# Performance work log

Measured on AMD Instinct MI355X. Metric: run time of the kernel, lower is better.

Reference implementation:

```python
import jax, jax.numpy as jnp
import numpy as np

RF = 500_000   # total full-rec atoms (rows)
F1 = 256       # input feature dim
NF = 128       # n_feat output dim
RA = 50_000    # number of residues (segments) = res_index.max()+1
LN_EPS = 1e-5


def setup_inputs() -> dict:
    key = jax.random.key(0)
    ks = jax.random.split(key, 5)
    full_rec_data = jax.random.normal(ks[0], (RF, F1), dtype=jnp.float32)
    # ensure segment RA-1 appears so amax()+1 == RA deterministically
    res_index = jax.random.randint(ks[1], (RF,), 0, RA, dtype=jnp.int32)
    res_index = res_index.at[0].set(RA - 1)
    W_feat = jax.random.normal(ks[2], (F1, NF), dtype=jnp.float32) * 0.05
    b_feat = jnp.zeros((NF,), dtype=jnp.float32)
    ln_gamma = jnp.ones((NF,), dtype=jnp.float32)
    ln_beta = jnp.zeros((NF,), dtype=jnp.float32)
    W_atn = jax.random.normal(ks[3], (F1, 1), dtype=jnp.float32) * 0.05
    b_atn = jnp.zeros((1,), dtype=jnp.float32)
    return {
        "full_rec_data": full_rec_data,
        "W_feat": W_feat,
        "b_feat": b_feat,
        "ln_gamma": ln_gamma,
        "ln_beta": ln_beta,
        "W_atn": W_atn,
        "b_atn": b_atn,
        "res_index": res_index,
        "n_feat": NF,
    }


def _layer_norm(x, gamma, beta):
    mu = jnp.mean(x, axis=-1, keepdims=True)
    var = jnp.mean(jnp.square(x - mu), axis=-1, keepdims=True)
    return (x - mu) * jax.lax.rsqrt(var + LN_EPS) * gamma + beta


def reference(full_rec_data, W_feat, b_feat, ln_gamma, ln_beta, W_atn, b_atn, res_index, n_feat):
    # NormAndLinear: LayerNorm(Linear(leaky_relu(x)))
    act = jax.nn.leaky_relu(full_rec_data, negative_slope=0.01)   # (Rf, F1)
    feat = _layer_norm(act @ W_feat + b_feat, ln_gamma, ln_beta)  # (Rf, NF)
    # attention logits (Rf, 1), globally max-stabilized as in the original
    atn = act @ W_atn + b_atn
    atn = jnp.exp(atn - jnp.max(atn))
    # segment softmax denominator; RA is static (res_index.amax()+1)
    atn_sum = jax.ops.segment_sum(atn, res_index, num_segments=RA)  # (Ra, 1)
    atn = atn / atn_sum[res_index]                                  # (Rf, 1)
    # weighted scatter-add pooling -> (Ra, NF)
    return jax.ops.segment_sum(feat * atn, res_index, num_segments=RA)
```

## Files before the change

### kernel.cpp

```cpp
#include <hip/hip_runtime.h>
#include <hip/hip_bf16.h>

#define RFn 500000
#define F1n 256
#define NFn 128
#define RAn 50000
#define LN_EPSn 1e-5f
#define RECB 256
#define LTS 272
#define NTILE (RFn / 16)
#define NWAVE 4096
#define ROWPAD 1040
#define BUFB (16 * ROWPAD)
#define SCB 256
#define SCG ((RAn + SCB - 1) / SCB)

typedef float f32x4 __attribute__((ext_vector_type(4)));
typedef short short8 __attribute__((ext_vector_type(8)));

__device__ __forceinline__ short f2bf(float f) {
  __hip_bfloat16 h = __float2bfloat16(f);
  return __builtin_bit_cast(short, h);
}

__device__ __forceinline__ void gload_lds16(const void* g, void* l) {
  __builtin_amdgcn_global_load_lds(
      (const __attribute__((address_space(1))) void*)g,
      (__attribute__((address_space(3))) void*)l, 16, 0, 0);
}

__global__ void prep_kernel(const float* __restrict__ Wf, short* __restrict__ frag) {
  int p = blockIdx.x * blockDim.x + threadIdx.x;
  if (p >= 4096) return;
  int f = p >> 6, l = p & 63;
  int s = f >> 3, c = f & 7;
  int col = c * 16 + (l & 15);
  int k0 = s * 32 + ((l >> 4) << 3);
  short8 v;
#pragma unroll
  for (int i = 0; i < 8; ++i) v[i] = f2bf(Wf[(k0 + i) * NFn + col]);
  *(short8*)(frag + (size_t)p * 8) = v;
}

__global__ void hist_kernel(const int* __restrict__ ri, int* __restrict__ hist) {
  int i = blockIdx.x * 256 + threadIdx.x;
  if (i < RFn) atomicAdd(&hist[ri[i]], 1);
}

__global__ __launch_bounds__(256) void scanA_kernel(const int* __restrict__ hist,
                                                    int* __restrict__ T,
                                                    int* __restrict__ bsum) {
  __shared__ int ls[256];
  const int t = threadIdx.x, idx = blockIdx.x * 256 + t;
  const int v = (idx < RAn) ? hist[idx] : 0;
  ls[t] = v;
  __syncthreads();
  for (int off = 1; off < 256; off <<= 1) {
    int add = (t >= off) ? ls[t - off] : 0;
    __syncthreads();
    ls[t] += add;
    __syncthreads();
  }
  if (idx < RAn) T[idx] = ls[t] - v;
  if (t == 255) bsum[blockIdx.x] = ls[255];
}

__global__ __launch_bounds__(256) void scanB_kernel(int* __restrict__ bsum,
                                                    int* __restrict__ boff) {
  __shared__ int ls[256];
  const int t = threadIdx.x;
  const int v = (t < SCG) ? bsum[t] : 0;
  ls[t] = v;
  __syncthreads();
  for (int off = 1; off < 256; off <<= 1) {
    int add = (t >= off) ? ls[t - off] : 0;
    __syncthreads();
    ls[t] += add;
    __syncthreads();
  }
  if (t < SCG) boff[t] = ls[t] - v;
}

__global__ __launch_bounds__(256) void scanC_kernel(const int* __restrict__ T,
                                                    const int* __restrict__ boff,
                                                    int* __restrict__ rowstart,
                                                    int* __restrict__ cursor) {
  const int idx = blockIdx.x * 256 + threadIdx.x;
  if (idx < RAn) {
    int v = T[idx] + boff[blockIdx.x];
    rowstart[idx] = v;
    cursor[idx] = v;
  }
  if (idx == 0) rowstart[RAn] = RFn;
}

__global__ void scatter_kernel(const int* __restrict__ ri, int* __restrict__ cursor,
                               int* __restrict__ inv) {
  int i = blockIdx.x * 256 + threadIdx.x;
  if (i < RFn) inv[i] = atomicAdd(&cursor[ri[i]], 1);
}

__global__ __launch_bounds__(64) void featw2_kernel(
    const float* __restrict__ X, const short* __restrict__ fragWS,
    const float* __restrict__ Wa, const float* __restrict__ ba,
    const float* __restrict__ bfeat, const float* __restrict__ gamma,
    const float* __restrict__ beta, const int* __restrict__ inv,
    char* __restrict__ buf, float* __restrict__ wbuf) {
  __shared__ __attribute__((aligned(16))) char lds[2 * BUFB];

  const int lane = threadIdx.x;
  const int colb = lane & 15;
  const int kg = lane >> 4;

  float g_r[8], be_r[8], bi_r[8];
#pragma unroll
  for (int c = 0; c < 8; ++c) {
    int col = c * 16 + colb;
    g_r[c] = gamma[col];
    be_r[c] = beta[col];
    bi_r[c] = bfeat[col];
  }
  const float batn = ba[0];

  int t = blockIdx.x;
  {
    const float* xr = X + (size_t)t * 16 * F1n;
#pragma unroll
    for (int r = 0; r < 16; ++r)
      gload_lds16(xr + r * F1n + lane * 4, &lds[r * ROWPAD]);
  }
  int cur = 0;

  while (true) {
    const int tn = t + NWAVE;
    const bool more = (tn < NTILE);

    asm volatile("s_waitcnt vmcnt(0)" ::: "memory");
    __builtin_amdgcn_sched_barrier(0);

    if (more) {
      const float* xr = X + (size_t)tn * 16 * F1n;
      char* db = &lds[(cur ^ 1) * BUFB];
#pragma unroll
      for (int r = 0; r < 16; ++r)
        gload_lds16(xr + r * F1n + lane * 4, db + r * ROWPAD);
    }

    const char* A = &lds[cur * BUFB];
    f32x4 acc[8];
#pragma unroll
    for (int c = 0; c < 8; ++c) acc[c] = (f32x4)(0.0f);
    float logit = 0.f;

#pragma unroll
    for (int s = 0; s < 8; ++s) {
      short8 bfr[8];
#pragma unroll
      for (int c = 0; c < 8; ++c)
        bfr[c] = *(const short8*)(fragWS + (((s * 8 + c) * 64 + lane) * 8));
      const float4 wa0 = *(const float4*)(Wa + s * 32 + kg * 8);
      const float4 wa1 = *(const float4*)(Wa + s * 32 + kg * 8 + 4);
      const float4 x0 = *(const float4*)(A + colb * ROWPAD + s * 128 + kg * 32);
      const float4 x1 = *(const float4*)(A + colb * ROWPAD + s * 128 + kg * 32 + 16);
      float a0 = fmaxf(x0.x, 0.01f * x0.x);
      float a1 = fmaxf(x0.y, 0.01f * x0.y);
      float a2 = fmaxf(x0.z, 0.01f * x0.z);
      float a3 = fmaxf(x0.w, 0.01f * x0.w);
      float a4 = fmaxf(x1.x, 0.01f * x1.x);
      float a5 = fmaxf(x1.y, 0.01f * x1.y);
      float a6 = fmaxf(x1.z, 0.01f * x1.z);
      float a7 = fmaxf(x1.w, 0.01f * x1.w);
      logit += a0 * wa0.x + a1 * wa0.y + a2 * wa0.z + a3 * wa0.w +
               a4 * wa1.x + a5 * wa1.y + a6 * wa1.z + a7 * wa1.w;
      short8 af;
      af[0] = f2bf(a0); af[1] = f2bf(a1); af[2] = f2bf(a2); af[3] = f2bf(a3);
      af[4] = f2bf(a4); af[5] = f2bf(a5); af[6] = f2bf(a6); af[7] = f2bf(a7);
#pragma unroll
      for (int c = 0; c < 8; ++c)
        acc[c] = __builtin_amdgcn_mfma_f32_16x16x32_bf16(af, bfr[c], acc[c], 0, 0, 0);
    }

    char* lt = &lds[cur * BUFB];
    {
      float lg = logit;
      lg += __shfl_xor(lg, 16);
      lg += __shfl_xor(lg, 32);
      const float wexp = __expf(lg + batn);
      if (lane < 16) wbuf[inv[t * 16 + colb]] = wexp;

      float w4[4];
#pragma unroll
      for (int reg = 0; reg < 4; ++reg) w4[reg] = __shfl(wexp, kg * 4 + reg);

      float s1v[4] = {0.f, 0.f, 0.f, 0.f}, s2v[4] = {0.f, 0.f, 0.f, 0.f};
#pragma unroll
      for (int c = 0; c < 8; ++c)
#pragma unroll
        for (int reg = 0; reg < 4; ++reg) {
          float v = acc[c][reg] + bi_r[c];
          acc[c][reg] = v;
          s1v[reg] += v;
          s2v[reg] += v * v;
        }
#pragma unroll
      for (int off = 1; off <= 8; off <<= 1)
#pragma unroll
        for (int reg = 0; reg < 4; ++reg) {
          s1v[reg] += __shfl_xor(s1v[reg], off);
          s2v[reg] += __shfl_xor(s2v[reg], off);
        }
#pragma unroll
      for (int reg = 0; reg < 4; ++reg) {
        float mu = s1v[reg] * (1.0f / NFn);
        float var = s2v[reg] * (1.0f / NFn) - mu * mu;
        float rs = rsqrtf(var + LN_EPSn);
#pragma unroll
        for (int c = 0; c < 8; ++c) {
          float feat = (acc[c][reg] - mu) * rs * g_r[c] + be_r[c];
          ((short*)lt)[(kg * 4 + reg) * (LTS / 2) + c * 16 + colb] =
              f2bf(feat * w4[reg]);
        }
      }
    }

    {
      const int r = lane >> 2, j = lane & 3;
      char* dst = buf + (size_t)inv[t * 16 + r] * RECB;
#pragma unroll
      for (int i = 0; i < 4; ++i) {
        int4 v = *(const int4*)&lt[r * LTS + j * 64 + i * 16];
        *(int4*)(dst + j * 64 + i * 16) = v;
      }
    }

    if (!more) break;
    cur ^= 1;
    t = tn;
  }
}

__global__ __launch_bounds__(256) void reduce_kernel(
    const char* __restrict__ buf, const float* __restrict__ wbuf,
    const int* __restrict__ rowstart, float* __restrict__ out) {
  const int lane = threadIdx.x & 63;
  const int seg = blockIdx.x * 4 + (threadIdx.x >> 6);
  if (seg >= RAn) return;
  const int rb = rowstart[seg], re = rowstart[seg + 1];
  float a0 = 0.f, a1 = 0.f, wsum = 0.f;
  for (int p = rb; p < re; ++p) {
    const char* rec = buf + (size_t)p * RECB;
    unsigned v = *(const unsigned*)(rec + lane * 4);
    a0 += __builtin_bit_cast(float, v << 16);
    a1 += __builtin_bit_cast(float, v & 0xffff0000u);
    wsum += wbuf[p];
  }
  float2 o;
  if (re > rb) {
    o.x = a0 / wsum;
    o.y = a1 / wsum;
  } else {
    o.x = 0.f;
    o.y = 0.f;
  }
  *(float2*)(out + (size_t)seg * NFn + lane * 2) = o;
}

__global__ __launch_bounds__(256) void main_atomic(
    const float* __restrict__ X, const short* __restrict__ fragWS,
    const float* __restrict__ Wa, const float* __restrict__ ba,
    const float* __restrict__ bfeat, const float* __restrict__ gamma,
    const float* __restrict__ beta, const int* __restrict__ res_index,
    float* __restrict__ Nacc, float* __restrict__ D) {
  __shared__ short sB[4096 * 8];
  const int tid = threadIdx.x;
  {
    const int4* src = (const int4*)fragWS;
    int4* dst = (int4*)sB;
#pragma unroll 4
    for (int i = tid; i < 4096; i += 256) dst[i] = src[i];
  }
  __syncthreads();
  const int lane = tid & 63;
  const int wv = tid >> 6;
  const int rowbase = blockIdx.x * 128 + wv * 32;
  const int colb = lane & 15;
  const int kg = lane >> 4;
  float g_r[8], be_r[8], bi_r[8];
#pragma unroll
  for (int c = 0; c < 8; ++c) {
    int col = c * 16 + colb;
    g_r[c] = gamma[col];
    be_r[c] = beta[col];
    bi_r[c] = bfeat[col];
  }
  const float batn = ba[0];
  f32x4 acc[2][8];
#pragma unroll
  for (int rt = 0; rt < 2; ++rt)
#pragma unroll
    for (int c = 0; c < 8; ++c) acc[rt][c] = (f32x4)(0.0f);
  float logit[2] = {0.f, 0.f};
  int gr0 = rowbase + colb;
  int gr1 = gr0 + 16;
  long r0 = (gr0 < RFn) ? gr0 : (RFn - 1);
  long r1 = (gr1 < RFn) ? gr1 : (RFn - 1);
  const float* xp0 = X + r0 * F1n + kg * 8;
  const float* xp1 = X + r1 * F1n + kg * 8;
#pragma unroll
  for (int s = 0; s < 8; ++s) {
    short8 bfr[8];
#pragma unroll
    for (int c = 0; c < 8; ++c)
      bfr[c] = *(const short8*)(sB + (((s * 8 + c) * 64 + lane) * 8));
    const float4 wa0 = *(const float4*)(Wa + s * 32 + kg * 8);
    const float4 wa1 = *(const float4*)(Wa + s * 32 + kg * 8 + 4);
#pragma unroll
    for (int rt = 0; rt < 2; ++rt) {
      const float* xp = rt ? xp1 : xp0;
      const float4 x0 = *(const float4*)(xp + s * 32);
      const float4 x1 = *(const float4*)(xp + s * 32 + 4);
      float a0 = fmaxf(x0.x, 0.01f * x0.x);
      float a1 = fmaxf(x0.y, 0.01f * x0.y);
      float a2 = fmaxf(x0.z, 0.01f * x0.z);
      float a3 = fmaxf(x0.w, 0.01f * x0.w);
      float a4 = fmaxf(x1.x, 0.01f * x1.x);
      float a5 = fmaxf(x1.y, 0.01f * x1.y);
      float a6 = fmaxf(x1.z, 0.01f * x1.z);
      float a7 = fmaxf(x1.w, 0.01f * x1.w);
      logit[rt] += a0 * wa0.x + a1 * wa0.y + a2 * wa0.z + a3 * wa0.w +
                   a4 * wa1.x + a5 * wa1.y + a6 * wa1.z + a7 * wa1.w;
      short8 af;
      af[0] = f2bf(a0); af[1] = f2bf(a1); af[2] = f2bf(a2); af[3] = f2bf(a3);
      af[4] = f2bf(a4); af[5] = f2bf(a5); af[6] = f2bf(a6); af[7] = f2bf(a7);
#pragma unroll
      for (int c = 0; c < 8; ++c)
        acc[rt][c] = __builtin_amdgcn_mfma_f32_16x16x32_bf16(af, bfr[c],
                                                             acc[rt][c], 0, 0, 0);
    }
  }
#pragma unroll
  for (int rt = 0; rt < 2; ++rt) {
    float lg = logit[rt];
    lg += __shfl_xor(lg, 16);
    lg += __shfl_xor(lg, 32);
    const float wexp = __expf(lg + batn);
    const int gr = rowbase + rt * 16 + colb;
    const int seg = res_index[(gr < RFn) ? gr : (RFn - 1)];
    if (lane < 16 && gr < RFn) atomicAdd(&D[seg], wexp);
    float w4[4];
    int s4[4], v4[4];
#pragma unroll
    for (int reg = 0; reg < 4; ++reg) {
      int srcl = kg * 4 + reg;
      w4[reg] = __shfl(wexp, srcl);
      s4[reg] = __shfl(seg, srcl);
      v4[reg] = (rowbase + rt * 16 + srcl) < RFn;
    }
    float s1v[4] = {0.f, 0.f, 0.f, 0.f}, s2v[4] = {0.f, 0.f, 0.f, 0.f};
#pragma unroll
    for (int c = 0; c < 8; ++c)
#pragma unroll
      for (int reg = 0; reg < 4; ++reg) {
        float t2 = acc[rt][c][reg] + bi_r[c];
        acc[rt][c][reg] = t2;
        s1v[reg] += t2;
        s2v[reg] += t2 * t2;
      }
#pragma unroll
    for (int off = 1; off <= 8; off <<= 1)
#pragma unroll
      for (int reg = 0; reg < 4; ++reg) {
        s1v[reg] += __shfl_xor(s1v[reg], off);
        s2v[reg] += __shfl_xor(s2v[reg], off);
      }
    float mu[4], rs[4];
#pragma unroll
    for (int reg = 0; reg < 4; ++reg) {
      mu[reg] = s1v[reg] * (1.0f / NFn);
      float var = s2v[reg] * (1.0f / NFn) - mu[reg] * mu[reg];
      rs[reg] = rsqrtf(var + LN_EPSn);
    }
#pragma unroll
    for (int c = 0; c < 8; ++c)
#pragma unroll
      for (int reg = 0; reg < 4; ++reg) {
        if (v4[reg]) {
          float feat = (acc[rt][c][reg] - mu[reg]) * rs[reg] * g_r[c] + be_r[c];
          atomicAdd(Nacc + (size_t)s4[reg] * NFn + c * 16 + colb, feat * w4[reg]);
        }
      }
  }
}

__global__ void div_kernel(float* __restrict__ out, const float* __restrict__ D) {
  int i = blockIdx.x * 256 + threadIdx.x;
  if (i < RAn * NFn) {
    float d = D[i >> 7];
    out[i] = (d > 0.f) ? out[i] / d : 0.f;
  }
}

extern "C" void kernel_launch(void* const* d_in, const int* in_sizes, int n_in,
                              void* d_out, int out_size, void* d_ws, size_t ws_size,
                              hipStream_t stream) {
  const float* X = (const float*)d_in[0];
  const float* Wf = (const float*)d_in[1];
  const float* bfeat = (const float*)d_in[2];
  const float* gamma = (const float*)d_in[3];
  const float* beta = (const float*)d_in[4];
  const float* Wa = (const float*)d_in[5];
  const float* ba = (const float*)d_in[6];
  const int* ri = (const int*)d_in[7];
  float* out = (float*)d_out;

  char* ws = (char*)d_ws;
  short* frag = (short*)ws;

  int* hist = (int*)(ws + 65536);
  int* T = (int*)(ws + 265536);
  int* bsum = (int*)(ws + 465536);
  int* boff = (int*)(ws + 466320);
  int* rowstart = (int*)(ws + 467104);
  int* cursor = (int*)(ws + 667108);
  int* inv = (int*)(ws + 867108);
  float* wbuf = (float*)(ws + 2867108);
  char* buf = ws + 4867328;
  const size_t NEED = 4867328ULL + (size_t)RFn * RECB;

  prep_kernel<<<16, 256, 0, stream>>>(Wf, frag);

  if (ws_size >= NEED) {
    hipMemsetAsync(hist, 0, (size_t)RAn * sizeof(int), stream);
    hist_kernel<<<(RFn + 255) / 256, 256, 0, stream>>>(ri, hist);
    scanA_kernel<<<SCG, 256, 0, stream>>>(hist, T, bsum);
    scanB_kernel<<<1, 256, 0, stream>>>(bsum, boff);
    scanC_kernel<<<SCG, 256, 0, stream>>>(T, boff, rowstart, cursor);
    scatter_kernel<<<(RFn + 255) / 256, 256, 0, stream>>>(ri, cursor, inv);
    featw2_kernel<<<NWAVE, 64, 0, stream>>>(X, frag, Wa, ba, bfeat, gamma, beta,
                                            inv, buf, wbuf);
    reduce_kernel<<<(RAn + 3) / 4, 256, 0, stream>>>(buf, wbuf, rowstart, out);
  } else {
    float* D = (float*)(ws + 65536);
    hipMemsetAsync(out, 0, (size_t)RAn * NFn * sizeof(float), stream);
    hipMemsetAsync(D, 0, (size_t)RAn * sizeof(float), stream);
    main_atomic<<<(RFn + 127) / 128, 256, 0, stream>>>(X, frag, Wa, ba, bfeat,
                                                       gamma, beta, ri, out, D);
    div_kernel<<<(RAn * NFn + 255) / 256, 256, 0, stream>>>(out, D);
  }
}
```

Baseline: 328.4 us.

## Replace persistent single-wave feature kernel with 512-thread blocks sharing LDS weights

Replaces the persistent 64-thread kernel, which double-buffered X tiles into LDS through direct global-to-LDS loads, with a 512-thread kernel. Each block stages the bf16 weight fragments in LDS once and each wave handles 32 rows, loading X straight from global memory. The MFMA operands are swapped so each lane holds a row's consecutive columns, which lets LayerNorm reduce with two shuffles and write records directly without an LDS transpose. The reduce kernel now processes two rows per wave with wider loads. The trade-off is dropping the explicit prefetch pipeline in favour of occupancy and weight reuse, with scattered 8-byte record stores.

```diff
diff --git a/kernel.cpp b/kernel.cpp
--- a/kernel.cpp
+++ b/kernel.cpp
@@ -7,11 +7,7 @@
 #define RAn 50000
 #define LN_EPSn 1e-5f
 #define RECB 256
-#define LTS 272
-#define NTILE (RFn / 16)
-#define NWAVE 4096
-#define ROWPAD 1040
-#define BUFB (16 * ROWPAD)
+#define BROWS 256
 #define SCB 256
 #define SCG ((RAn + SCB - 1) / SCB)
 
@@ -21,12 +17,6 @@
 __device__ __forceinline__ short f2bf(float f) {
   __hip_bfloat16 h = __float2bfloat16(f);
   return __builtin_bit_cast(short, h);
-}
-
-__device__ __forceinline__ void gload_lds16(const void* g, void* l) {
-  __builtin_amdgcn_global_load_lds(
-      (const __attribute__((address_space(1))) void*)g,
-      (__attribute__((address_space(3))) void*)l, 16, 0, 0);
 }
 
 __global__ void prep_kernel(const float* __restrict__ Wf, short* __restrict__ frag) {
@@ -100,212 +90,52 @@
   if (i < RFn) inv[i] = atomicAdd(&cursor[ri[i]], 1);
 }
 
-__global__ __launch_bounds__(64) void featw2_kernel(
+__global__ __launch_bounds__(512, 4) void featw3_kernel(
     const float* __restrict__ X, const short* __restrict__ fragWS,
     const float* __restrict__ Wa, const float* __restrict__ ba,
     const float* __restrict__ bfeat, const float* __restrict__ gamma,
     const float* __restrict__ beta, const int* __restrict__ inv,
     char* __restrict__ buf, float* __restrict__ wbuf) {
-  __shared__ __attribute__((aligned(16))) char lds[2 * BUFB];
-
-  const int lane = threadIdx.x;
-  const int colb = lane & 15;
-  const int kg = lane >> 4;
-
-  float g_r[8], be_r[8], bi_r[8];
-#pragma unroll
-  for (int c = 0; c < 8; ++c) {
-    int col = c * 16 + colb;
-    g_r[c] = gamma[col];
-    be_r[c] = beta[col];
-    bi_r[c] = bfeat[col];
-  }
-  const float batn = ba[0];
-
-  int t = blockIdx.x;
-  {
-    const float* xr = X + (size_t)t * 16 * F1n;
-#pragma unroll
-    for (int r = 0; r < 16; ++r)
-      gload_lds16(xr + r * F1n + lane * 4, &lds[r * ROWPAD]);
-  }
-  int cur = 0;
-
-  while (true) {
-    const int tn = t + NWAVE;
-    const bool more = (tn < NTILE);
-
-    asm volatile("s_waitcnt vmcnt(0)" ::: "memory");
-    __builtin_amdgcn_sched_barrier(0);
-
-    if (more) {
-      const float* xr = X + (size_t)tn * 16 * F1n;
-      char* db = &lds[(cur ^ 1) * BUFB];
-#pragma unroll
-      for (int r = 0; r < 16; ++r)
-        gload_lds16(xr + r * F1n + lane * 4, db + r * ROWPAD);
-    }
-
-    const char* A = &lds[cur * BUFB];
-    f32x4 acc[8];
-#pragma unroll
-    for (int c = 0; c < 8; ++c) acc[c] = (f32x4)(0.0f);
-    float logit = 0.f;
-
-#pragma unroll
-    for (int s = 0; s < 8; ++s) {
-      short8 bfr[8];
-#pragma unroll
-      for (int c = 0; c < 8; ++c)
-        bfr[c] = *(const short8*)(fragWS + (((s * 8 + c) * 64 + lane) * 8));
-      const float4 wa0 = *(const float4*)(Wa + s * 32 + kg * 8);
-      const float4 wa1 = *(const float4*)(Wa + s * 32 + kg * 8 + 4);
-      const float4 x0 = *(const float4*)(A + colb * ROWPAD + s * 128 + kg * 32);
-      const float4 x1 = *(const float4*)(A + colb * ROWPAD + s * 128 + kg * 32 + 16);
-      float a0 = fmaxf(x0.x, 0.01f * x0.x);
-      float a1 = fmaxf(x0.y, 0.01f * x0.y);
-      float a2 = fmaxf(x0.z, 0.01f * x0.z);
-      float a3 = fmaxf(x0.w, 0.01f * x0.w);
-      float a4 = fmaxf(x1.x, 0.01f * x1.x);
-      float a5 = fmaxf(x1.y, 0.01f * x1.y);
-      float a6 = fmaxf(x1.z, 0.01f * x1.z);
-      float a7 = fmaxf(x1.w, 0.01f * x1.w);
-      logit += a0 * wa0.x + a1 * wa0.y + a2 * wa0.z + a3 * wa0.w +
-               a4 * wa1.x + a5 * wa1.y + a6 * wa1.z + a7 * wa1.w;
-      short8 af;
-      af[0] = f2bf(a0); af[1] = f2bf(a1); af[2] = f2bf(a2); af[3] = f2bf(a3);
-      af[4] = f2bf(a4); af[5] = f2bf(a5); af[6] = f2bf(a6); af[7] = f2bf(a7);
-#pragma unroll
-      for (int c = 0; c < 8; ++c)
-        acc[c] = __builtin_amdgcn_mfma_f32_16x16x32_bf16(af, bfr[c], acc[c], 0, 0, 0);
-    }
-
-    char* lt = &lds[cur * BUFB];
-    {
-      float lg = logit;
-      lg += __shfl_xor(lg, 16);
-      lg += __shfl_xor(lg, 32);
-      const float wexp = __expf(lg + batn);
-      if (lane < 16) wbuf[inv[t * 16 + colb]] = wexp;
-
-      float w4[4];
-#pragma unroll
-      for (int reg = 0; reg < 4; ++reg) w4[reg] = __shfl(wexp, kg * 4 + reg);
-
-      float s1v[4] = {0.f, 0.f, 0.f, 0.f}, s2v[4] = {0.f, 0.f, 0.f, 0.f};
-#pragma unroll
-      for (int c = 0; c < 8; ++c)
-#pragma unroll
-        for (int reg = 0; reg < 4; ++reg) {
-          float v = acc[c][reg] + bi_r[c];
-          acc[c][reg] = v;
-          s1v[reg] += v;
-          s2v[reg] += v * v;
-        }
-#pragma unroll
-      for (int off = 1; off <= 8; off <<= 1)
-#pragma unroll
-        for (int reg = 0; reg < 4; ++reg) {
-          s1v[reg] += __shfl_xor(s1v[reg], off);
-          s2v[reg] += __shfl_xor(s2v[reg], off);
-        }
-#pragma unroll
-      for (int reg = 0; reg < 4; ++reg) {
-        float mu = s1v[reg] * (1.0f / NFn);
-        float var = s2v[reg] * (1.0f / NFn) - mu * mu;
-        float rs = rsqrtf(var + LN_EPSn);
-#pragma unroll
-        for (int c = 0; c < 8; ++c) {
-          float feat = (acc[c][reg] - mu) * rs * g_r[c] + be_r[c];
-          ((short*)lt)[(kg * 4 + reg) * (LTS / 2) + c * 16 + colb] =
-              f2bf(feat * w4[reg]);
-        }
-      }
-    }
-
-    {
-      const int r = lane >> 2, j = lane & 3;
-      char* dst = buf + (size_t)inv[t * 16 + r] * RECB;
-#pragma unroll
-      for (int i = 0; i < 4; ++i) {
-        int4 v = *(const int4*)&lt[r * LTS + j * 64 + i * 16];
-        *(int4*)(dst + j * 64 + i * 16) = v;
-      }
-    }
-
-    if (!more) break;
-    cur ^= 1;
-    t = tn;
-  }
-}
-
-__global__ __launch_bounds__(256) void reduce_kernel(
-    const char* __restrict__ buf, const float* __restrict__ wbuf,
-    const int* __restrict__ rowstart, float* __restrict__ out) {
-  const int lane = threadIdx.x & 63;
-  const int seg = blockIdx.x * 4 + (threadIdx.x >> 6);
-  if (seg >= RAn) return;
-  const int rb = rowstart[seg], re = rowstart[seg + 1];
-  float a0 = 0.f, a1 = 0.f, wsum = 0.f;
-  for (int p = rb; p < re; ++p) {
-    const char* rec = buf + (size_t)p * RECB;
-    unsigned v = *(const unsigned*)(rec + lane * 4);
-    a0 += __builtin_bit_cast(float, v << 16);
-    a1 += __builtin_bit_cast(float, v & 0xffff0000u);
-    wsum += wbuf[p];
-  }
-  float2 o;
-  if (re > rb) {
-    o.x = a0 / wsum;
-    o.y = a1 / wsum;
-  } else {
-    o.x = 0.f;
-    o.y = 0.f;
-  }
-  *(float2*)(out + (size_t)seg * NFn + lane * 2) = o;
-}
-
-__global__ __launch_bounds__(256) void main_atomic(
-    const float* __restrict__ X, const short* __restrict__ fragWS,
-    const float* __restrict__ Wa, const float* __restrict__ ba,
-    const float* __restrict__ bfeat, const float* __restrict__ gamma,
-    const float* __restrict__ beta, const int* __restrict__ res_index,
-    float* __restrict__ Nacc, float* __restrict__ D) {
   __shared__ short sB[4096 * 8];
+
   const int tid = threadIdx.x;
   {
     const int4* src = (const int4*)fragWS;
     int4* dst = (int4*)sB;
-#pragma unroll 4
-    for (int i = tid; i < 4096; i += 256) dst[i] = src[i];
+#pragma unroll 8
+    for (int i = tid; i < 4096; i += 512) dst[i] = src[i];
   }
   __syncthreads();
+
   const int lane = tid & 63;
   const int wv = tid >> 6;
-  const int rowbase = blockIdx.x * 128 + wv * 32;
   const int colb = lane & 15;
   const int kg = lane >> 4;
-  float g_r[8], be_r[8], bi_r[8];
+  const int rowbase = blockIdx.x * BROWS + wv * 32;
+
+  f32x4 g4[8], be4[8], bi4[8];
 #pragma unroll
   for (int c = 0; c < 8; ++c) {
-    int col = c * 16 + colb;
-    g_r[c] = gamma[col];
-    be_r[c] = beta[col];
-    bi_r[c] = bfeat[col];
+    g4[c] = *(const f32x4*)(gamma + c * 16 + kg * 4);
+    be4[c] = *(const f32x4*)(beta + c * 16 + kg * 4);
+    bi4[c] = *(const f32x4*)(bfeat + c * 16 + kg * 4);
   }
   const float batn = ba[0];
+
   f32x4 acc[2][8];
 #pragma unroll
   for (int rt = 0; rt < 2; ++rt)
 #pragma unroll
     for (int c = 0; c < 8; ++c) acc[rt][c] = (f32x4)(0.0f);
   float logit[2] = {0.f, 0.f};
-  int gr0 = rowbase + colb;
-  int gr1 = gr0 + 16;
-  long r0 = (gr0 < RFn) ? gr0 : (RFn - 1);
-  long r1 = (gr1 < RFn) ? gr1 : (RFn - 1);
+
+  const int gr0 = rowbase + colb;
+  const int gr1 = gr0 + 16;
+  const long r0 = (gr0 < RFn) ? gr0 : (RFn - 1);
+  const long r1 = (gr1 < RFn) ? gr1 : (RFn - 1);
   const float* xp0 = X + r0 * F1n + kg * 8;
   const float* xp1 = X + r1 * F1n + kg * 8;
+
 #pragma unroll
   for (int s = 0; s < 8; ++s) {
     short8 bfr[8];
@@ -334,6 +164,164 @@
       af[4] = f2bf(a4); af[5] = f2bf(a5); af[6] = f2bf(a6); af[7] = f2bf(a7);
 #pragma unroll
       for (int c = 0; c < 8; ++c)
+        acc[rt][c] =
+            __builtin_amdgcn_mfma_f32_16x16x32_bf16(bfr[c], af, acc[rt][c], 0, 0, 0);
+    }
+  }
+
+#pragma unroll
+  for (int rt = 0; rt < 2; ++rt) {
+    float lg = logit[rt];
+    lg += __shfl_xor(lg, 16);
+    lg += __shfl_xor(lg, 32);
+    const float wexp = __expf(lg + batn);
+
+    const int gr = rowbase + rt * 16 + colb;
+    const bool valid = (gr < RFn);
+    const int pos = inv[valid ? gr : (RFn - 1)];
+    if (valid && lane < 16) wbuf[pos] = wexp;
+
+    float s1 = 0.f, s2 = 0.f;
+#pragma unroll
+    for (int c = 0; c < 8; ++c)
+#pragma unroll
+      for (int j = 0; j < 4; ++j) {
+        float v = acc[rt][c][j] + bi4[c][j];
+        acc[rt][c][j] = v;
+        s1 += v;
+        s2 += v * v;
+      }
+    s1 += __shfl_xor(s1, 16);
+    s1 += __shfl_xor(s1, 32);
+    s2 += __shfl_xor(s2, 16);
+    s2 += __shfl_xor(s2, 32);
+    const float mu = s1 * (1.0f / NFn);
+    const float var = s2 * (1.0f / NFn) - mu * mu;
+    const float rs = rsqrtf(var + LN_EPSn);
+
+    if (valid) {
+      char* rec = buf + (size_t)pos * RECB + kg * 8;
+#pragma unroll
+      for (int c = 0; c < 8; ++c) {
+        short4 o;
+        o.x = f2bf(((acc[rt][c][0] - mu) * rs * g4[c][0] + be4[c][0]) * wexp);
+        o.y = f2bf(((acc[rt][c][1] - mu) * rs * g4[c][1] + be4[c][1]) * wexp);
+        o.z = f2bf(((acc[rt][c][2] - mu) * rs * g4[c][2] + be4[c][2]) * wexp);
+        o.w = f2bf(((acc[rt][c][3] - mu) * rs * g4[c][3] + be4[c][3]) * wexp);
+        *(short4*)(rec + c * 32) = o;
+      }
+    }
+  }
+}
+
+__global__ __launch_bounds__(256) void reduce_kernel(
+    const char* __restrict__ buf, const float* __restrict__ wbuf,
+    const int* __restrict__ rowstart, float* __restrict__ out) {
+  const int lane = threadIdx.x & 63;
+  const int seg = blockIdx.x * 4 + (threadIdx.x >> 6);
+  if (seg >= RAn) return;
+  const int rb = rowstart[seg], re = rowstart[seg + 1];
+  const int h = lane >> 5;
+  const int sl = lane & 31;
+  float a0 = 0.f, a1 = 0.f, a2 = 0.f, a3 = 0.f, ws = 0.f;
+  for (int base = rb; base < re; base += 2) {
+    const int p = base + h;
+    if (p < re) {
+      const char* rec = buf + (size_t)p * RECB;
+      uint2 v = *(const uint2*)(rec + sl * 8);
+      a0 += __builtin_bit_cast(float, v.x << 16);
+      a1 += __builtin_bit_cast(float, v.x & 0xffff0000u);
+      a2 += __builtin_bit_cast(float, v.y << 16);
+      a3 += __builtin_bit_cast(float, v.y & 0xffff0000u);
+      ws += wbuf[p];
+    }
+  }
+  a0 += __shfl_xor(a0, 32);
+  a1 += __shfl_xor(a1, 32);
+  a2 += __shfl_xor(a2, 32);
+  a3 += __shfl_xor(a3, 32);
+  ws += __shfl_xor(ws, 32);
+  if (h == 0) {
+    float4 o;
+    if (re > rb) {
+      const float iw = 1.0f / ws;
+      o.x = a0 * iw; o.y = a1 * iw; o.z = a2 * iw; o.w = a3 * iw;
+    } else {
+      o.x = o.y = o.z = o.w = 0.f;
+    }
+    *(float4*)(out + (size_t)seg * NFn + sl * 4) = o;
+  }
+}
+
+__global__ __launch_bounds__(256) void main_atomic(
+    const float* __restrict__ X, const short* __restrict__ fragWS,
+    const float* __restrict__ Wa, const float* __restrict__ ba,
+    const float* __restrict__ bfeat, const float* __restrict__ gamma,
+    const float* __restrict__ beta, const int* __restrict__ res_index,
+    float* __restrict__ Nacc, float* __restrict__ D) {
+  __shared__ short sB[4096 * 8];
+  const int tid = threadIdx.x;
+  {
+    const int4* src = (const int4*)fragWS;
+    int4* dst = (int4*)sB;
+#pragma unroll 4
+    for (int i = tid; i < 4096; i += 256) dst[i] = src[i];
+  }
+  __syncthreads();
+  const int lane = tid & 63;
+  const int wv = tid >> 6;
+  const int rowbase = blockIdx.x * 128 + wv * 32;
+  const int colb = lane & 15;
+  const int kg = lane >> 4;
+  float g_r[8], be_r[8], bi_r[8];
+#pragma unroll
+  for (int c = 0; c < 8; ++c) {
+    int col = c * 16 + colb;
+    g_r[c] = gamma[col];
+    be_r[c] = beta[col];
+    bi_r[c] = bfeat[col];
+  }
+  const float batn = ba[0];
+  f32x4 acc[2][8];
+#pragma unroll
+  for (int rt = 0; rt < 2; ++rt)
+#pragma unroll
+    for (int c = 0; c < 8; ++c) acc[rt][c] = (f32x4)(0.0f);
+  float logit[2] = {0.f, 0.f};
+  int gr0 = rowbase + colb;
+  int gr1 = gr0 + 16;
+  long r0 = (gr0 < RFn) ? gr0 : (RFn - 1);
+  long r1 = (gr1 < RFn) ? gr1 : (RFn - 1);
+  const float* xp0 = X + r0 * F1n + kg * 8;
+  const float* xp1 = X + r1 * F1n + kg * 8;
+#pragma unroll
+  for (int s = 0; s < 8; ++s) {
+    short8 bfr[8];
+#pragma unroll
+    for (int c = 0; c < 8; ++c)
+      bfr[c] = *(const short8*)(sB + (((s * 8 + c) * 64 + lane) * 8));
+    const float4 wa0 = *(const float4*)(Wa + s * 32 + kg * 8);
+    const float4 wa1 = *(const float4*)(Wa + s * 32 + kg * 8 + 4);
+#pragma unroll
+    for (int rt = 0; rt < 2; ++rt) {
+      const float* xp = rt ? xp1 : xp0;
+      const float4 x0 = *(const float4*)(xp + s * 32);
+      const float4 x1 = *(const float4*)(xp + s * 32 + 4);
+      float a0 = fmaxf(x0.x, 0.01f * x0.x);
+      float a1 = fmaxf(x0.y, 0.01f * x0.y);
+      float a2 = fmaxf(x0.z, 0.01f * x0.z);
+      float a3 = fmaxf(x0.w, 0.01f * x0.w);
+      float a4 = fmaxf(x1.x, 0.01f * x1.x);
+      float a5 = fmaxf(x1.y, 0.01f * x1.y);
+      float a6 = fmaxf(x1.z, 0.01f * x1.z);
+      float a7 = fmaxf(x1.w, 0.01f * x1.w);
+      logit[rt] += a0 * wa0.x + a1 * wa0.y + a2 * wa0.z + a3 * wa0.w +
+                   a4 * wa1.x + a5 * wa1.y + a6 * wa1.z + a7 * wa1.w;
+      short8 af;
+      af[0] = f2bf(a0); af[1] = f2bf(a1); af[2] = f2bf(a2); af[3] = f2bf(a3);
+      af[4] = f2bf(a4); af[5] = f2bf(a5); af[6] = f2bf(a6); af[7] = f2bf(a7);
+#pragma unroll
+      for (int c = 0; c < 8; ++c)
         acc[rt][c] = __builtin_amdgcn_mfma_f32_16x16x32_bf16(af, bfr[c],
                                                              acc[rt][c], 0, 0, 0);
     }
@@ -436,8 +424,8 @@
     scanB_kernel<<<1, 256, 0, stream>>>(bsum, boff);
     scanC_kernel<<<SCG, 256, 0, stream>>>(T, boff, rowstart, cursor);
     scatter_kernel<<<(RFn + 255) / 256, 256, 0, stream>>>(ri, cursor, inv);
-    featw2_kernel<<<NWAVE, 64, 0, stream>>>(X, frag, Wa, ba, bfeat, gamma, beta,
-                                            inv, buf, wbuf);
+    featw3_kernel<<<(RFn + BROWS - 1) / BROWS, 512, 0, stream>>>(
+        X, frag, Wa, ba, bfeat, gamma, beta, inv, buf, wbuf);
     reduce_kernel<<<(RAn + 3) / 4, 256, 0, stream>>>(buf, wbuf, rowstart, out);
   } else {
     float* D = (float*)(ws + 65536);
```

New measurement: 728.5 us. 2.22x slower.

## Fuse feature compute and segment reduction using sorted-row gather per wave

Applied to the files above, without the earlier changes.

Replaces the feature kernel that wrote bf16 per-row records to a scratch buffer plus a separate reduce kernel with one fused kernel. Each wave owns five consecutive segments, gathers their rows through a sorted permutation, computes GEMM, LayerNorm and weights, and accumulates per-segment sums in registers before writing the output directly. This removes the large intermediate buffer write and read and keeps the W fragments in LDS. In exchange, X rows are gathered at random addresses without the async LDS prefetch, and work per wave varies with segment sizes.

```diff
diff --git a/kernel.cpp b/kernel.cpp
--- a/kernel.cpp
+++ b/kernel.cpp
@@ -6,12 +6,9 @@
 #define NFn 128
 #define RAn 50000
 #define LN_EPSn 1e-5f
-#define RECB 256
-#define LTS 272
-#define NTILE (RFn / 16)
-#define NWAVE 4096
-#define ROWPAD 1040
-#define BUFB (16 * ROWPAD)
+#define SPW 5
+#define NWV ((RAn + SPW - 1) / SPW)
+#define NBLK2 ((NWV + 7) / 8)
 #define SCB 256
 #define SCG ((RAn + SCB - 1) / SCB)
 
@@ -21,12 +18,6 @@
 __device__ __forceinline__ short f2bf(float f) {
   __hip_bfloat16 h = __float2bfloat16(f);
   return __builtin_bit_cast(short, h);
-}
-
-__device__ __forceinline__ void gload_lds16(const void* g, void* l) {
-  __builtin_amdgcn_global_load_lds(
-      (const __attribute__((address_space(1))) void*)g,
-      (__attribute__((address_space(3))) void*)l, 16, 0, 0);
 }
 
 __global__ void prep_kernel(const float* __restrict__ Wf, short* __restrict__ frag) {
@@ -95,22 +86,46 @@
 }
 
 __global__ void scatter_kernel(const int* __restrict__ ri, int* __restrict__ cursor,
-                               int* __restrict__ inv) {
+                               int* __restrict__ perm, int* __restrict__ sseg) {
   int i = blockIdx.x * 256 + threadIdx.x;
-  if (i < RFn) inv[i] = atomicAdd(&cursor[ri[i]], 1);
-}
-
-__global__ __launch_bounds__(64) void featw2_kernel(
+  if (i < RFn) {
+    int s = ri[i];
+    int pos = atomicAdd(&cursor[s], 1);
+    perm[pos] = i;
+    sseg[pos] = s;
+  }
+}
+
+__global__ __launch_bounds__(512, 2) void fused_kernel(
     const float* __restrict__ X, const short* __restrict__ fragWS,
     const float* __restrict__ Wa, const float* __restrict__ ba,
     const float* __restrict__ bfeat, const float* __restrict__ gamma,
-    const float* __restrict__ beta, const int* __restrict__ inv,
-    char* __restrict__ buf, float* __restrict__ wbuf) {
-  __shared__ __attribute__((aligned(16))) char lds[2 * BUFB];
-
-  const int lane = threadIdx.x;
+    const float* __restrict__ beta, const int* __restrict__ rowstart,
+    const int* __restrict__ perm, const int* __restrict__ sseg,
+    float* __restrict__ out) {
+  __shared__ short sB[4096 * 8];
+
+  const int tid = threadIdx.x;
+  {
+    const int4* src = (const int4*)fragWS;
+    int4* dst = (int4*)sB;
+#pragma unroll 8
+    for (int i = tid; i < 4096; i += 512) dst[i] = src[i];
+  }
+  __syncthreads();
+
+  const int lane = tid & 63;
+  const int wv = tid >> 6;
   const int colb = lane & 15;
   const int kg = lane >> 4;
+
+  const int wgid = blockIdx.x * 8 + wv;
+  const int s0 = wgid * SPW;
+  if (s0 >= RAn) return;
+  const int s1 = min(s0 + SPW, RAn);
+  const int rbeg = rowstart[s0];
+  const int rend = rowstart[s1];
+  if (rend <= rbeg) return;
 
   float g_r[8], be_r[8], bi_r[8];
 #pragma unroll
@@ -122,31 +137,17 @@
   }
   const float batn = ba[0];
 
-  int t = blockIdx.x;
-  {
-    const float* xr = X + (size_t)t * 16 * F1n;
-#pragma unroll
-    for (int r = 0; r < 16; ++r)
-      gload_lds16(xr + r * F1n + lane * 4, &lds[r * ROWPAD]);
-  }
-  int cur = 0;
-
-  while (true) {
-    const int tn = t + NWAVE;
-    const bool more = (tn < NTILE);
-
-    asm volatile("s_waitcnt vmcnt(0)" ::: "memory");
-    __builtin_amdgcn_sched_barrier(0);
-
-    if (more) {
-      const float* xr = X + (size_t)tn * 16 * F1n;
-      char* db = &lds[(cur ^ 1) * BUFB];
-#pragma unroll
-      for (int r = 0; r < 16; ++r)
-        gload_lds16(xr + r * F1n + lane * 4, db + r * ROWPAD);
-    }
-
-    const char* A = &lds[cur * BUFB];
+  float racc[8] = {0.f, 0.f, 0.f, 0.f, 0.f, 0.f, 0.f, 0.f};
+  float wrun = 0.f;
+  int curseg = -1;
+
+  for (int base = rbeg; base < rend; base += 16) {
+    const int n = min(16, rend - base);
+    const int pc = base + ((colb < n) ? colb : (n - 1));
+    const int row = perm[pc];
+    const int seg = sseg[pc];
+    const float* xp = X + (size_t)row * F1n + kg * 8;
+
     f32x4 acc[8];
 #pragma unroll
     for (int c = 0; c < 8; ++c) acc[c] = (f32x4)(0.0f);
@@ -157,11 +158,11 @@
       short8 bfr[8];
 #pragma unroll
       for (int c = 0; c < 8; ++c)
-        bfr[c] = *(const short8*)(fragWS + (((s * 8 + c) * 64 + lane) * 8));
+        bfr[c] = *(const short8*)(sB + (((s * 8 + c) * 64 + lane) * 8));
       const float4 wa0 = *(const float4*)(Wa + s * 32 + kg * 8);
       const float4 wa1 = *(const float4*)(Wa + s * 32 + kg * 8 + 4);
-      const float4 x0 = *(const float4*)(A + colb * ROWPAD + s * 128 + kg * 32);
-      const float4 x1 = *(const float4*)(A + colb * ROWPAD + s * 128 + kg * 32 + 16);
+      const float4 x0 = *(const float4*)(xp + s * 32);
+      const float4 x1 = *(const float4*)(xp + s * 32 + 4);
       float a0 = fmaxf(x0.x, 0.01f * x0.x);
       float a1 = fmaxf(x0.y, 0.01f * x0.y);
       float a2 = fmaxf(x0.z, 0.01f * x0.z);
@@ -180,89 +181,100 @@
         acc[c] = __builtin_amdgcn_mfma_f32_16x16x32_bf16(af, bfr[c], acc[c], 0, 0, 0);
     }
 
-    char* lt = &lds[cur * BUFB];
-    {
-      float lg = logit;
-      lg += __shfl_xor(lg, 16);
-      lg += __shfl_xor(lg, 32);
-      const float wexp = __expf(lg + batn);
-      if (lane < 16) wbuf[inv[t * 16 + colb]] = wexp;
-
-      float w4[4];
-#pragma unroll
-      for (int reg = 0; reg < 4; ++reg) w4[reg] = __shfl(wexp, kg * 4 + reg);
-
-      float s1v[4] = {0.f, 0.f, 0.f, 0.f}, s2v[4] = {0.f, 0.f, 0.f, 0.f};
+    float lg = logit;
+    lg += __shfl_xor(lg, 16);
+    lg += __shfl_xor(lg, 32);
+    const float wexp = __expf(lg + batn);
+
+    float w4[4];
+#pragma unroll
+    for (int reg = 0; reg < 4; ++reg) w4[reg] = __shfl(wexp, kg * 4 + reg);
+
+    float s1v[4] = {0.f, 0.f, 0.f, 0.f}, s2v[4] = {0.f, 0.f, 0.f, 0.f};
+#pragma unroll
+    for (int c = 0; c < 8; ++c)
+#pragma unroll
+      for (int reg = 0; reg < 4; ++reg) {
+        float v = acc[c][reg] + bi_r[c];
+        acc[c][reg] = v;
+        s1v[reg] += v;
+        s2v[reg] += v * v;
+      }
+#pragma unroll
+    for (int off = 1; off <= 8; off <<= 1)
+#pragma unroll
+      for (int reg = 0; reg < 4; ++reg) {
+        s1v[reg] += __shfl_xor(s1v[reg], off);
+        s2v[reg] += __shfl_xor(s2v[reg], off);
+      }
+#pragma unroll
+    for (int reg = 0; reg < 4; ++reg) {
+      const float mu = s1v[reg] * (1.0f / NFn);
+      const float var = s2v[reg] * (1.0f / NFn) - mu * mu;
+      const float rs = rsqrtf(var + LN_EPSn);
 #pragma unroll
       for (int c = 0; c < 8; ++c)
-#pragma unroll
-        for (int reg = 0; reg < 4; ++reg) {
-          float v = acc[c][reg] + bi_r[c];
-          acc[c][reg] = v;
-          s1v[reg] += v;
-          s2v[reg] += v * v;
+        acc[c][reg] = ((acc[c][reg] - mu) * rs * g_r[c] + be_r[c]) * w4[reg];
+    }
+
+    const int lm1 = (lane & 15) ? lane - 1 : lane;
+    const int segp = __shfl(seg, lm1 & 63);
+    unsigned long long bm =
+        __ballot(lane < n && ((lane & 15) == 0 || seg != segp));
+    bm &= 0xFFFFull;
+
+    int a = 0;
+    while (a < n) {
+      unsigned long long rest = (a + 1 < 16) ? (bm >> (a + 1)) : 0ull;
+      const int b = rest ? (a + 1 + (int)__builtin_ctzll(rest)) : n;
+      const int rseg = __shfl(seg, a);
+
+      float ctr[8];
+#pragma unroll
+      for (int c = 0; c < 8; ++c) ctr[c] = 0.f;
+      float wc = 0.f;
+#pragma unroll
+      for (int reg = 0; reg < 4; ++reg) {
+        const int r = kg * 4 + reg;
+        if (r >= a && r < b) {
+          wc += w4[reg];
+#pragma unroll
+          for (int c = 0; c < 8; ++c) ctr[c] += acc[c][reg];
         }
-#pragma unroll
-      for (int off = 1; off <= 8; off <<= 1)
-#pragma unroll
-        for (int reg = 0; reg < 4; ++reg) {
-          s1v[reg] += __shfl_xor(s1v[reg], off);
-          s2v[reg] += __shfl_xor(s2v[reg], off);
+      }
+#pragma unroll
+      for (int c = 0; c < 8; ++c) {
+        ctr[c] += __shfl_xor(ctr[c], 16);
+        ctr[c] += __shfl_xor(ctr[c], 32);
+      }
+      wc += __shfl_xor(wc, 16);
+      wc += __shfl_xor(wc, 32);
+
+      if (rseg != curseg) {
+        if (curseg >= 0) {
+          const float iw = 1.0f / wrun;
+          out[(size_t)curseg * NFn + (2 * kg) * 16 + colb] = racc[2 * kg] * iw;
+          out[(size_t)curseg * NFn + (2 * kg + 1) * 16 + colb] =
+              racc[2 * kg + 1] * iw;
         }
-#pragma unroll
-      for (int reg = 0; reg < 4; ++reg) {
-        float mu = s1v[reg] * (1.0f / NFn);
-        float var = s2v[reg] * (1.0f / NFn) - mu * mu;
-        float rs = rsqrtf(var + LN_EPSn);
-#pragma unroll
-        for (int c = 0; c < 8; ++c) {
-          float feat = (acc[c][reg] - mu) * rs * g_r[c] + be_r[c];
-          ((short*)lt)[(kg * 4 + reg) * (LTS / 2) + c * 16 + colb] =
-              f2bf(feat * w4[reg]);
-        }
-      }
-    }
-
-    {
-      const int r = lane >> 2, j = lane & 3;
-      char* dst = buf + (size_t)inv[t * 16 + r] * RECB;
-#pragma unroll
-      for (int i = 0; i < 4; ++i) {
-        int4 v = *(const int4*)&lt[r * LTS + j * 64 + i * 16];
-        *(int4*)(dst + j * 64 + i * 16) = v;
-      }
-    }
-
-    if (!more) break;
-    cur ^= 1;
-    t = tn;
-  }
-}
-
-__global__ __launch_bounds__(256) void reduce_kernel(
-    const char* __restrict__ buf, const float* __restrict__ wbuf,
-    const int* __restrict__ rowstart, float* __restrict__ out) {
-  const int lane = threadIdx.x & 63;
-  const int seg = blockIdx.x * 4 + (threadIdx.x >> 6);
-  if (seg >= RAn) return;
-  const int rb = rowstart[seg], re = rowstart[seg + 1];
-  float a0 = 0.f, a1 = 0.f, wsum = 0.f;
-  for (int p = rb; p < re; ++p) {
-    const char* rec = buf + (size_t)p * RECB;
-    unsigned v = *(const unsigned*)(rec + lane * 4);
-    a0 += __builtin_bit_cast(float, v << 16);
-    a1 += __builtin_bit_cast(float, v & 0xffff0000u);
-    wsum += wbuf[p];
-  }
-  float2 o;
-  if (re > rb) {
-    o.x = a0 / wsum;
-    o.y = a1 / wsum;
-  } else {
-    o.x = 0.f;
-    o.y = 0.f;
-  }
-  *(float2*)(out + (size_t)seg * NFn + lane * 2) = o;
+        curseg = rseg;
+#pragma unroll
+        for (int c = 0; c < 8; ++c) racc[c] = ctr[c];
+        wrun = wc;
+      } else {
+#pragma unroll
+        for (int c = 0; c < 8; ++c) racc[c] += ctr[c];
+        wrun += wc;
+      }
+      a = b;
+    }
+  }
+
+  if (curseg >= 0) {
+    const float iw = 1.0f / wrun;
+    out[(size_t)curseg * NFn + (2 * kg) * 16 + colb] = racc[2 * kg] * iw;
+    out[(size_t)curseg * NFn + (2 * kg + 1) * 16 + colb] = racc[2 * kg + 1] * iw;
+  }
 }
 
 __global__ __launch_bounds__(256) void main_atomic(
@@ -415,19 +427,18 @@
 
   char* ws = (char*)d_ws;
   short* frag = (short*)ws;
-
   int* hist = (int*)(ws + 65536);
   int* T = (int*)(ws + 265536);
   int* bsum = (int*)(ws + 465536);
   int* boff = (int*)(ws + 466320);
   int* rowstart = (int*)(ws + 467104);
   int* cursor = (int*)(ws + 667108);
-  int* inv = (int*)(ws + 867108);
-  float* wbuf = (float*)(ws + 2867108);
-  char* buf = ws + 4867328;
-  const size_t NEED = 4867328ULL + (size_t)RFn * RECB;
+  int* perm = (int*)(ws + 867108);
+  int* sseg = (int*)(ws + 2867108);
+  const size_t NEED = 4867108ULL;
 
   prep_kernel<<<16, 256, 0, stream>>>(Wf, frag);
+  hipMemsetAsync(out, 0, (size_t)RAn * NFn * sizeof(float), stream);
 
   if (ws_size >= NEED) {
     hipMemsetAsync(hist, 0, (size_t)RAn * sizeof(int), stream);
@@ -435,13 +446,11 @@
     scanA_kernel<<<SCG, 256, 0, stream>>>(hist, T, bsum);
     scanB_kernel<<<1, 256, 0, stream>>>(bsum, boff);
     scanC_kernel<<<SCG, 256, 0, stream>>>(T, boff, rowstart, cursor);
-    scatter_kernel<<<(RFn + 255) / 256, 256, 0, stream>>>(ri, cursor, inv);
-    featw2_kernel<<<NWAVE, 64, 0, stream>>>(X, frag, Wa, ba, bfeat, gamma, beta,
-                                            inv, buf, wbuf);
-    reduce_kernel<<<(RAn + 3) / 4, 256, 0, stream>>>(buf, wbuf, rowstart, out);
+    scatter_kernel<<<(RFn + 255) / 256, 256, 0, stream>>>(ri, cursor, perm, sseg);
+    fused_kernel<<<NBLK2, 512, 0, stream>>>(X, frag, Wa, ba, bfeat, gamma, beta,
+                                            rowstart, perm, sseg, out);
   } else {
     float* D = (float*)(ws + 65536);
-    hipMemsetAsync(out, 0, (size_t)RAn * NFn * sizeof(float), stream);
     hipMemsetAsync(D, 0, (size_t)RAn * sizeof(float), stream);
     main_atomic<<<(RFn + 127) / 128, 256, 0, stream>>>(X, frag, Wa, ba, bfeat,
                                                        gamma, beta, ri, out, D);
```

New measurement: 738.3 us. +124.8%, slower.

## Split feature tile across two waves per block, drop persistent double-buffered loop

Applied to the files above, without the earlier changes.

The feature kernel now launches one 128-thread block per 16-row tile. Each of its two waves computes half of the 128 output columns and shares LayerNorm partial sums through LDS. This replaces the persistent single-wave kernel that double-buffered its X loads in LDS. The aim is to halve per-wave MFMA work and weight-fragment register pressure and to raise occupancy, but it gives up the explicit load/compute overlap and adds block barriers.

```diff
diff --git a/kernel.cpp b/kernel.cpp
--- a/kernel.cpp
+++ b/kernel.cpp
@@ -7,11 +7,8 @@
 #define RAn 50000
 #define LN_EPSn 1e-5f
 #define RECB 256
-#define LTS 272
 #define NTILE (RFn / 16)
-#define NWAVE 4096
 #define ROWPAD 1040
-#define BUFB (16 * ROWPAD)
 #define SCB 256
 #define SCG ((RAn + SCB - 1) / SCB)
 
@@ -100,142 +97,139 @@
   if (i < RFn) inv[i] = atomicAdd(&cursor[ri[i]], 1);
 }
 
-__global__ __launch_bounds__(64) void featw2_kernel(
+__global__ __launch_bounds__(128) void featw4_kernel(
     const float* __restrict__ X, const short* __restrict__ fragWS,
     const float* __restrict__ Wa, const float* __restrict__ ba,
     const float* __restrict__ bfeat, const float* __restrict__ gamma,
     const float* __restrict__ beta, const int* __restrict__ inv,
     char* __restrict__ buf, float* __restrict__ wbuf) {
-  __shared__ __attribute__((aligned(16))) char lds[2 * BUFB];
-
-  const int lane = threadIdx.x;
+  __shared__ __attribute__((aligned(16))) char lt[16 * ROWPAD];
+  __shared__ float sLN[2][16][2];
+
+  const int tid = threadIdx.x;
+  const int lane = tid & 63;
+  const int wv = tid >> 6;
   const int colb = lane & 15;
   const int kg = lane >> 4;
-
-  float g_r[8], be_r[8], bi_r[8];
-#pragma unroll
-  for (int c = 0; c < 8; ++c) {
-    int col = c * 16 + colb;
-    g_r[c] = gamma[col];
-    be_r[c] = beta[col];
-    bi_r[c] = bfeat[col];
-  }
-  const float batn = ba[0];
-
-  int t = blockIdx.x;
+  const int t = blockIdx.x;
+
   {
     const float* xr = X + (size_t)t * 16 * F1n;
 #pragma unroll
-    for (int r = 0; r < 16; ++r)
-      gload_lds16(xr + r * F1n + lane * 4, &lds[r * ROWPAD]);
-  }
-  int cur = 0;
-
-  while (true) {
-    const int tn = t + NWAVE;
-    const bool more = (tn < NTILE);
-
-    asm volatile("s_waitcnt vmcnt(0)" ::: "memory");
-    __builtin_amdgcn_sched_barrier(0);
-
-    if (more) {
-      const float* xr = X + (size_t)tn * 16 * F1n;
-      char* db = &lds[(cur ^ 1) * BUFB];
-#pragma unroll
-      for (int r = 0; r < 16; ++r)
-        gload_lds16(xr + r * F1n + lane * 4, db + r * ROWPAD);
-    }
-
-    const char* A = &lds[cur * BUFB];
-    f32x4 acc[8];
-#pragma unroll
-    for (int c = 0; c < 8; ++c) acc[c] = (f32x4)(0.0f);
-    float logit = 0.f;
-
-#pragma unroll
-    for (int s = 0; s < 8; ++s) {
-      short8 bfr[8];
-#pragma unroll
-      for (int c = 0; c < 8; ++c)
-        bfr[c] = *(const short8*)(fragWS + (((s * 8 + c) * 64 + lane) * 8));
-      const float4 wa0 = *(const float4*)(Wa + s * 32 + kg * 8);
-      const float4 wa1 = *(const float4*)(Wa + s * 32 + kg * 8 + 4);
-      const float4 x0 = *(const float4*)(A + colb * ROWPAD + s * 128 + kg * 32);
-      const float4 x1 = *(const float4*)(A + colb * ROWPAD + s * 128 + kg * 32 + 16);
-      float a0 = fmaxf(x0.x, 0.01f * x0.x);
-      float a1 = fmaxf(x0.y, 0.01f * x0.y);
-      float a2 = fmaxf(x0.z, 0.01f * x0.z);
-      float a3 = fmaxf(x0.w, 0.01f * x0.w);
-      float a4 = fmaxf(x1.x, 0.01f * x1.x);
-      float a5 = fmaxf(x1.y, 0.01f * x1.y);
-      float a6 = fmaxf(x1.z, 0.01f * x1.z);
-      float a7 = fmaxf(x1.w, 0.01f * x1.w);
-      logit += a0 * wa0.x + a1 * wa0.y + a2 * wa0.z + a3 * wa0.w +
-               a4 * wa1.x + a5 * wa1.y + a6 * wa1.z + a7 * wa1.w;
-      short8 af;
-      af[0] = f2bf(a0); af[1] = f2bf(a1); af[2] = f2bf(a2); af[3] = f2bf(a3);
-      af[4] = f2bf(a4); af[5] = f2bf(a5); af[6] = f2bf(a6); af[7] = f2bf(a7);
-#pragma unroll
-      for (int c = 0; c < 8; ++c)
-        acc[c] = __builtin_amdgcn_mfma_f32_16x16x32_bf16(af, bfr[c], acc[c], 0, 0, 0);
-    }
-
-    char* lt = &lds[cur * BUFB];
-    {
-      float lg = logit;
-      lg += __shfl_xor(lg, 16);
-      lg += __shfl_xor(lg, 32);
-      const float wexp = __expf(lg + batn);
-      if (lane < 16) wbuf[inv[t * 16 + colb]] = wexp;
-
-      float w4[4];
-#pragma unroll
-      for (int reg = 0; reg < 4; ++reg) w4[reg] = __shfl(wexp, kg * 4 + reg);
-
-      float s1v[4] = {0.f, 0.f, 0.f, 0.f}, s2v[4] = {0.f, 0.f, 0.f, 0.f};
-#pragma unroll
-      for (int c = 0; c < 8; ++c)
-#pragma unroll
-        for (int reg = 0; reg < 4; ++reg) {
-          float v = acc[c][reg] + bi_r[c];
-          acc[c][reg] = v;
-          s1v[reg] += v;
-          s2v[reg] += v * v;
-        }
-#pragma unroll
-      for (int off = 1; off <= 8; off <<= 1)
-#pragma unroll
-        for (int reg = 0; reg < 4; ++reg) {
-          s1v[reg] += __shfl_xor(s1v[reg], off);
-          s2v[reg] += __shfl_xor(s2v[reg], off);
-        }
-#pragma unroll
-      for (int reg = 0; reg < 4; ++reg) {
-        float mu = s1v[reg] * (1.0f / NFn);
-        float var = s2v[reg] * (1.0f / NFn) - mu * mu;
-        float rs = rsqrtf(var + LN_EPSn);
-#pragma unroll
-        for (int c = 0; c < 8; ++c) {
-          float feat = (acc[c][reg] - mu) * rs * g_r[c] + be_r[c];
-          ((short*)lt)[(kg * 4 + reg) * (LTS / 2) + c * 16 + colb] =
-              f2bf(feat * w4[reg]);
-        }
-      }
-    }
-
-    {
-      const int r = lane >> 2, j = lane & 3;
-      char* dst = buf + (size_t)inv[t * 16 + r] * RECB;
-#pragma unroll
-      for (int i = 0; i < 4; ++i) {
-        int4 v = *(const int4*)&lt[r * LTS + j * 64 + i * 16];
-        *(int4*)(dst + j * 64 + i * 16) = v;
-      }
-    }
-
-    if (!more) break;
-    cur ^= 1;
-    t = tn;
+    for (int r = 0; r < 8; ++r) {
+      const int rr = wv * 8 + r;
+      gload_lds16(xr + rr * F1n + lane * 4, &lt[rr * ROWPAD]);
+    }
+  }
+
+  float g_r[4], be_r[4], bi_r[4];
+#pragma unroll
+  for (int cc = 0; cc < 4; ++cc) {
+    const int col = (wv * 4 + cc) * 16 + colb;
+    g_r[cc] = gamma[col];
+    be_r[cc] = beta[col];
+    bi_r[cc] = bfeat[col];
+  }
+  const float batn = ba[0];
+
+  __syncthreads();
+
+  f32x4 acc[4];
+#pragma unroll
+  for (int cc = 0; cc < 4; ++cc) acc[cc] = (f32x4)(0.0f);
+  float logit = 0.f;
+
+#pragma unroll
+  for (int s = 0; s < 8; ++s) {
+    short8 bfr[4];
+#pragma unroll
+    for (int cc = 0; cc < 4; ++cc)
+      bfr[cc] = *(const short8*)(fragWS + (((s * 8 + wv * 4 + cc) * 64 + lane) * 8));
+    const float4 wa0 = *(const float4*)(Wa + s * 32 + kg * 8);
+    const float4 wa1 = *(const float4*)(Wa + s * 32 + kg * 8 + 4);
+    const float4 x0 = *(const float4*)(lt + colb * ROWPAD + s * 128 + kg * 32);
+    const float4 x1 = *(const float4*)(lt + colb * ROWPAD + s * 128 + kg * 32 + 16);
+    float a0 = fmaxf(x0.x, 0.01f * x0.x);
+    float a1 = fmaxf(x0.y, 0.01f * x0.y);
+    float a2 = fmaxf(x0.z, 0.01f * x0.z);
+    float a3 = fmaxf(x0.w, 0.01f * x0.w);
+    float a4 = fmaxf(x1.x, 0.01f * x1.x);
+    float a5 = fmaxf(x1.y, 0.01f * x1.y);
+    float a6 = fmaxf(x1.z, 0.01f * x1.z);
+    float a7 = fmaxf(x1.w, 0.01f * x1.w);
+    logit += a0 * wa0.x + a1 * wa0.y + a2 * wa0.z + a3 * wa0.w +
+             a4 * wa1.x + a5 * wa1.y + a6 * wa1.z + a7 * wa1.w;
+    short8 af;
+    af[0] = f2bf(a0); af[1] = f2bf(a1); af[2] = f2bf(a2); af[3] = f2bf(a3);
+    af[4] = f2bf(a4); af[5] = f2bf(a5); af[6] = f2bf(a6); af[7] = f2bf(a7);
+#pragma unroll
+    for (int cc = 0; cc < 4; ++cc)
+      acc[cc] = __builtin_amdgcn_mfma_f32_16x16x32_bf16(af, bfr[cc], acc[cc], 0, 0, 0);
+  }
+
+  float lg = logit;
+  lg += __shfl_xor(lg, 16);
+  lg += __shfl_xor(lg, 32);
+  const float wexp = __expf(lg + batn);
+  if (wv == 0 && lane < 16) wbuf[inv[t * 16 + colb]] = wexp;
+
+  float s1v[4] = {0.f, 0.f, 0.f, 0.f}, s2v[4] = {0.f, 0.f, 0.f, 0.f};
+#pragma unroll
+  for (int cc = 0; cc < 4; ++cc)
+#pragma unroll
+    for (int reg = 0; reg < 4; ++reg) {
+      const float v = acc[cc][reg] + bi_r[cc];
+      acc[cc][reg] = v;
+      s1v[reg] += v;
+      s2v[reg] += v * v;
+    }
+#pragma unroll
+  for (int off = 1; off <= 8; off <<= 1)
+#pragma unroll
+    for (int reg = 0; reg < 4; ++reg) {
+      s1v[reg] += __shfl_xor(s1v[reg], off);
+      s2v[reg] += __shfl_xor(s2v[reg], off);
+    }
+  if (colb == 0) {
+#pragma unroll
+    for (int reg = 0; reg < 4; ++reg) {
+      sLN[wv][kg * 4 + reg][0] = s1v[reg];
+      sLN[wv][kg * 4 + reg][1] = s2v[reg];
+    }
+  }
+  __syncthreads();
+
+  float w4[4];
+#pragma unroll
+  for (int reg = 0; reg < 4; ++reg) w4[reg] = __shfl(wexp, kg * 4 + reg);
+
+#pragma unroll
+  for (int reg = 0; reg < 4; ++reg) {
+    const int row = kg * 4 + reg;
+    const float s1 = s1v[reg] + sLN[wv ^ 1][row][0];
+    const float s2 = s2v[reg] + sLN[wv ^ 1][row][1];
+    const float mu = s1 * (1.0f / NFn);
+    const float var = s2 * (1.0f / NFn) - mu * mu;
+    const float rs = rsqrtf(var + LN_EPSn);
+#pragma unroll
+    for (int cc = 0; cc < 4; ++cc) {
+      const float feat = (acc[cc][reg] - mu) * rs * g_r[cc] + be_r[cc];
+      ((short*)lt)[row * (RECB / 2 + 8) + (wv * 4 + cc) * 16 + colb] =
+          f2bf(feat * w4[reg]);
+    }
+  }
+  __syncthreads();
+
+  {
+    const int row = wv * 8 + (lane >> 3);
+    const int p = lane & 7;
+    const int pos = inv[t * 16 + row];
+    const char* src = lt + row * 272 + p * 32;
+    char* dst = buf + (size_t)pos * RECB + p * 32;
+    int4 v0 = *(const int4*)(src);
+    int4 v1 = *(const int4*)(src + 16);
+    *(int4*)(dst) = v0;
+    *(int4*)(dst + 16) = v1;
   }
 }
 
@@ -415,7 +409,6 @@
 
   char* ws = (char*)d_ws;
   short* frag = (short*)ws;
-
   int* hist = (int*)(ws + 65536);
   int* T = (int*)(ws + 265536);
   int* bsum = (int*)(ws + 465536);
@@ -436,8 +429,8 @@
     scanB_kernel<<<1, 256, 0, stream>>>(bsum, boff);
     scanC_kernel<<<SCG, 256, 0, stream>>>(T, boff, rowstart, cursor);
     scatter_kernel<<<(RFn + 255) / 256, 256, 0, stream>>>(ri, cursor, inv);
-    featw2_kernel<<<NWAVE, 64, 0, stream>>>(X, frag, Wa, ba, bfeat, gamma, beta,
-                                            inv, buf, wbuf);
+    featw4_kernel<<<NTILE, 128, 0, stream>>>(X, frag, Wa, ba, bfeat, gamma,
+                                             beta, inv, buf, wbuf);
     reduce_kernel<<<(RAn + 3) / 4, 256, 0, stream>>>(buf, wbuf, rowstart, out);
   } else {
     float* D = (float*)(ws + 65536);
```

Result: faster. 308.7 us (-6.0%).
